# Kernel tuning notes

Measured on AMD Instinct MI355X. Metric: run time of the kernel, lower is better.

## Reference

```python
import jax, jax.numpy as jnp
import numpy as np

B = 8192
N = 1024


def euler_to_matrix_xyz(e):
    # e: [B,3] angles; R = Rx(a) @ Ry(b) @ Rz(c) (pytorch3d 'XYZ' convention)
    a, b, c = e[..., 0], e[..., 1], e[..., 2]
    ca, sa = jnp.cos(a), jnp.sin(a)
    cb, sb = jnp.cos(b), jnp.sin(b)
    cc, sc = jnp.cos(c), jnp.sin(c)
    one = jnp.ones_like(a)
    zero = jnp.zeros_like(a)
    Rx = jnp.stack([one, zero, zero,
                    zero, ca, -sa,
                    zero, sa, ca], axis=-1).reshape(-1, 3, 3)
    Ry = jnp.stack([cb, zero, sb,
                    zero, one, zero,
                    -sb, zero, cb], axis=-1).reshape(-1, 3, 3)
    Rz = jnp.stack([cc, -sc, zero,
                    sc, cc, zero,
                    zero, zero, one], axis=-1).reshape(-1, 3, 3)
    return jnp.einsum('bij,bjk->bik', Rx, jnp.einsum('bij,bjk->bik', Ry, Rz))


def manifold2euler(manifold, mode):
    m1, m2, m3, m4 = (manifold[:, 0], manifold[:, 1], manifold[:, 2], manifold[:, 3])
    sgn = jnp.where(mode > 0.5, 1.0, -1.0)
    euler2 = sgn * jnp.arcsin(jnp.sqrt(m3 ** 2 / (m1 ** 2 + m2 ** 2 + m3 ** 2)))
    euler3 = jnp.arctan2(m4, m3 / (jnp.sin(euler2) + 1e-9))
    tmp = jnp.cos(euler2) * jnp.cos(euler3)
    euler1 = jnp.arctan2(m2 / tmp, m1 / tmp)
    euler3 = jnp.where(euler3 > 0, euler3, euler3 + 2 * np.pi)
    return jnp.stack([euler1, euler2, euler3], axis=-1)


def setup_inputs() -> dict:
    key = jax.random.key(0)
    k1, k2, k3, k4 = jax.random.split(key, 4)
    return {
        'pred': jax.random.normal(k1, (B, 4), dtype=jnp.float32),
        'mode': jax.random.uniform(k2, (B,), dtype=jnp.float32),
        'gt': jax.random.normal(k3, (B, 3), dtype=jnp.float32),
        'point': jax.random.normal(k4, (B, N, 3), dtype=jnp.float32),
    }


def reference(pred, mode, gt, point):
    euler_pred = manifold2euler(pred, mode)          # [B,3]
    rm_gt = euler_to_matrix_xyz(gt)                  # [B,3,3]
    rm_pred = euler_to_matrix_xyz(euler_pred)        # [B,3,3]
    # original: row-vector point [*,1,3] @ R [*,3,3]; R depends only on batch
    point_gt = jnp.einsum('bnj,bjk->bnk', point, rm_gt)
    point_pred = jnp.einsum('bnj,bjk->bnk', point, rm_pred)
    diff = point_pred - point_gt                     # [B,N,3]
    dist = jnp.linalg.norm(diff, axis=-1)            # [B,N]
    return jnp.mean(dist)
```

## Files before the change

### kernel.cpp

```cpp
#include <hip/hip_runtime.h>
#include <math.h>

constexpr int B_ = 8192;
constexpr int N_ = 1024;
constexpr int NTHREADS = 256;
constexpr int BATCHES_PER_BLOCK = 4;
constexpr int NBLOCKS = B_ / BATCHES_PER_BLOCK;

__device__ __forceinline__ void euler_to_mat(float a, float b, float c, float R[9]) {
    float ca = cosf(a), sa = sinf(a);
    float cb = cosf(b), sb = sinf(b);
    float cc = cosf(c), sc = sinf(c);
    R[0] = cb * cc;             R[1] = -cb * sc;            R[2] = sb;
    R[3] = ca * sc + sa * sb * cc; R[4] = ca * cc - sa * sb * sc; R[5] = -sa * cb;
    R[6] = sa * sc - ca * sb * cc; R[7] = sa * cc + ca * sb * sc; R[8] = ca * cb;
}

__global__ __launch_bounds__(NTHREADS)
void add_loss_kernel(const float* __restrict__ pred,
                     const float* __restrict__ mode,
                     const float* __restrict__ gt,
                     const float* __restrict__ point,
                     float* __restrict__ out)
{
    __shared__ float sM[9];
    __shared__ float spts[N_ * 3];
    __shared__ float swave[NTHREADS / 64];

    const int tid = threadIdx.x;
    float local = 0.0f;

    for (int ib = 0; ib < BATCHES_PER_BLOCK; ++ib) {
        const int b = blockIdx.x * BATCHES_PER_BLOCK + ib;

        const float4* gp = (const float4*)(point + (size_t)b * (N_ * 3));
        float4* sp4 = (float4*)spts;
        #pragma unroll
        for (int i = 0; i < (N_ * 3 / 4) / NTHREADS; ++i)
            sp4[tid + NTHREADS * i] = gp[tid + NTHREADS * i];

        if (tid == 0) {
            float m1 = pred[b * 4 + 0], m2 = pred[b * 4 + 1];
            float m3 = pred[b * 4 + 2], m4 = pred[b * 4 + 3];
            float sgn = (mode[b] > 0.5f) ? 1.0f : -1.0f;
            float e2 = sgn * asinf(sqrtf(m3 * m3 / (m1 * m1 + m2 * m2 + m3 * m3)));
            float e3 = atan2f(m4, m3 / (sinf(e2) + 1e-9f));
            float tmp = cosf(e2) * cosf(e3);
            float e1 = atan2f(m2 / tmp, m1 / tmp);
            e3 = (e3 > 0.0f) ? e3 : (e3 + 6.2831854820251465f);
            float P[9], G[9];
            euler_to_mat(e1, e2, e3, P);
            euler_to_mat(gt[b * 3 + 0], gt[b * 3 + 1], gt[b * 3 + 2], G);
            #pragma unroll
            for (int i = 0; i < 9; ++i) sM[i] = P[i] - G[i];
        }
        __syncthreads();

        const float M0 = sM[0], M1 = sM[1], M2 = sM[2];
        const float M3 = sM[3], M4 = sM[4], M5 = sM[5];
        const float M6 = sM[6], M7 = sM[7], M8 = sM[8];

        #pragma unroll
        for (int i = 0; i < N_ / NTHREADS; ++i) {
            int n = tid + NTHREADS * i;
            float px = spts[3 * n + 0], py = spts[3 * n + 1], pz = spts[3 * n + 2];
            float dx = px * M0 + py * M3 + pz * M6;
            float dy = px * M1 + py * M4 + pz * M7;
            float dz = px * M2 + py * M5 + pz * M8;
            local += sqrtf(dx * dx + dy * dy + dz * dz);
        }
        __syncthreads();
    }

    #pragma unroll
    for (int off = 32; off > 0; off >>= 1)
        local += __shfl_down(local, off, 64);
    if ((tid & 63) == 0) swave[tid >> 6] = local;
    __syncthreads();
    if (tid == 0) {
        float s = swave[0] + swave[1] + swave[2] + swave[3];
        atomicAdd(out, s * (1.0f / ((float)B_ * (float)N_)));
    }
}

extern "C" void kernel_launch(void* const* d_in, const int* in_sizes, int n_in,
                              void* d_out, int out_size, void* d_ws, size_t ws_size,
                              hipStream_t stream) {
    const float* pred  = (const float*)d_in[0];
    const float* mode  = (const float*)d_in[1];
    const float* gt    = (const float*)d_in[2];
    const float* point = (const float*)d_in[3];
    float* out = (float*)d_out;

    hipMemsetAsync(out, 0, sizeof(float), stream);
    add_loss_kernel<<<NBLOCKS, NTHREADS, 0, stream>>>(pred, mode, gt, point, out);
}
```

Before: 171.2 us.

## Split rotation prep, per-batch point kernel, and deterministic two-stage reduction

Moves the per-batch rotation-difference matrix computation into a separate fully parallel prep kernel, so it no longer runs serially on one thread per block while the others wait. The point kernel now assigns one batch per block and loads points straight into registers as three float4 per thread, removing the shared-memory staging and its extra barriers. The global atomic is replaced by per-block partial sums and a single-block final reduction. This adds two extra kernel launches and a workspace round trip, and keeps a fused fallback for when the workspace is too small.

```diff
diff --git a/kernel.cpp b/kernel.cpp
--- a/kernel.cpp
+++ b/kernel.cpp
@@ -4,83 +4,132 @@
 constexpr int B_ = 8192;
 constexpr int N_ = 1024;
 constexpr int NTHREADS = 256;
-constexpr int BATCHES_PER_BLOCK = 4;
-constexpr int NBLOCKS = B_ / BATCHES_PER_BLOCK;
+constexpr float SCALE = 1.0f / ((float)B_ * (float)N_);
 
 __device__ __forceinline__ void euler_to_mat(float a, float b, float c, float R[9]) {
     float ca = cosf(a), sa = sinf(a);
     float cb = cosf(b), sb = sinf(b);
     float cc = cosf(c), sc = sinf(c);
-    R[0] = cb * cc;             R[1] = -cb * sc;            R[2] = sb;
+    R[0] = cb * cc;                R[1] = -cb * sc;               R[2] = sb;
     R[3] = ca * sc + sa * sb * cc; R[4] = ca * cc - sa * sb * sc; R[5] = -sa * cb;
     R[6] = sa * sc - ca * sb * cc; R[7] = sa * cc + ca * sb * sc; R[8] = ca * cb;
 }
 
+__device__ __forceinline__ void compute_M(const float* __restrict__ pred,
+                                          const float* __restrict__ mode,
+                                          const float* __restrict__ gt,
+                                          int b, float M[9]) {
+    float m1 = pred[b * 4 + 0], m2 = pred[b * 4 + 1];
+    float m3 = pred[b * 4 + 2], m4 = pred[b * 4 + 3];
+    float sgn = (mode[b] > 0.5f) ? 1.0f : -1.0f;
+    float e2 = sgn * asinf(sqrtf(m3 * m3 / (m1 * m1 + m2 * m2 + m3 * m3)));
+    float e3 = atan2f(m4, m3 / (sinf(e2) + 1e-9f));
+    float tmp = cosf(e2) * cosf(e3);
+    float e1 = atan2f(m2 / tmp, m1 / tmp);
+    e3 = (e3 > 0.0f) ? e3 : (e3 + 6.2831854820251465f);
+    float P[9], G[9];
+    euler_to_mat(e1, e2, e3, P);
+    euler_to_mat(gt[b * 3 + 0], gt[b * 3 + 1], gt[b * 3 + 2], G);
+    #pragma unroll
+    for (int i = 0; i < 9; ++i) M[i] = P[i] - G[i];
+}
+
+__global__ __launch_bounds__(256)
+void prep_M_kernel(const float* __restrict__ pred, const float* __restrict__ mode,
+                   const float* __restrict__ gt, float* __restrict__ Mout) {
+    int b = blockIdx.x * blockDim.x + threadIdx.x;
+    if (b >= B_) return;
+    float M[9];
+    compute_M(pred, mode, gt, b, M);
+    #pragma unroll
+    for (int i = 0; i < 9; ++i) Mout[b * 9 + i] = M[i];
+}
+
+__device__ __forceinline__ float dist3(float px, float py, float pz, const float M[9]) {
+    float dx = px * M[0] + py * M[3] + pz * M[6];
+    float dy = px * M[1] + py * M[4] + pz * M[7];
+    float dz = px * M[2] + py * M[5] + pz * M[8];
+    return sqrtf(dx * dx + dy * dy + dz * dz);
+}
+
 __global__ __launch_bounds__(NTHREADS)
-void add_loss_kernel(const float* __restrict__ pred,
-                     const float* __restrict__ mode,
-                     const float* __restrict__ gt,
-                     const float* __restrict__ point,
-                     float* __restrict__ out)
+void point_kernel(const float* __restrict__ point,
+                  const float* __restrict__ Mg,
+                  float* __restrict__ partial)
 {
+    const int b = blockIdx.x;
+    const int t = threadIdx.x;
     __shared__ float sM[9];
-    __shared__ float spts[N_ * 3];
     __shared__ float swave[NTHREADS / 64];
 
-    const int tid = threadIdx.x;
-    float local = 0.0f;
+    if (t < 9) sM[t] = Mg[b * 9 + t];
+    __syncthreads();
+    float M[9];
+    #pragma unroll
+    for (int i = 0; i < 9; ++i) M[i] = sM[i];
 
-    for (int ib = 0; ib < BATCHES_PER_BLOCK; ++ib) {
-        const int b = blockIdx.x * BATCHES_PER_BLOCK + ib;
+    const float4* gp = (const float4*)(point + (size_t)b * (N_ * 3));
+    float4 p0 = gp[3 * t + 0];
+    float4 p1 = gp[3 * t + 1];
+    float4 p2 = gp[3 * t + 2];
 
-        const float4* gp = (const float4*)(point + (size_t)b * (N_ * 3));
-        float4* sp4 = (float4*)spts;
-        #pragma unroll
-        for (int i = 0; i < (N_ * 3 / 4) / NTHREADS; ++i)
-            sp4[tid + NTHREADS * i] = gp[tid + NTHREADS * i];
-
-        if (tid == 0) {
-            float m1 = pred[b * 4 + 0], m2 = pred[b * 4 + 1];
-            float m3 = pred[b * 4 + 2], m4 = pred[b * 4 + 3];
-            float sgn = (mode[b] > 0.5f) ? 1.0f : -1.0f;
-            float e2 = sgn * asinf(sqrtf(m3 * m3 / (m1 * m1 + m2 * m2 + m3 * m3)));
-            float e3 = atan2f(m4, m3 / (sinf(e2) + 1e-9f));
-            float tmp = cosf(e2) * cosf(e3);
-            float e1 = atan2f(m2 / tmp, m1 / tmp);
-            e3 = (e3 > 0.0f) ? e3 : (e3 + 6.2831854820251465f);
-            float P[9], G[9];
-            euler_to_mat(e1, e2, e3, P);
-            euler_to_mat(gt[b * 3 + 0], gt[b * 3 + 1], gt[b * 3 + 2], G);
-            #pragma unroll
-            for (int i = 0; i < 9; ++i) sM[i] = P[i] - G[i];
-        }
-        __syncthreads();
-
-        const float M0 = sM[0], M1 = sM[1], M2 = sM[2];
-        const float M3 = sM[3], M4 = sM[4], M5 = sM[5];
-        const float M6 = sM[6], M7 = sM[7], M8 = sM[8];
-
-        #pragma unroll
-        for (int i = 0; i < N_ / NTHREADS; ++i) {
-            int n = tid + NTHREADS * i;
-            float px = spts[3 * n + 0], py = spts[3 * n + 1], pz = spts[3 * n + 2];
-            float dx = px * M0 + py * M3 + pz * M6;
-            float dy = px * M1 + py * M4 + pz * M7;
-            float dz = px * M2 + py * M5 + pz * M8;
-            local += sqrtf(dx * dx + dy * dy + dz * dz);
-        }
-        __syncthreads();
-    }
+    float local = dist3(p0.x, p0.y, p0.z, M)
+                + dist3(p0.w, p1.x, p1.y, M)
+                + dist3(p1.z, p1.w, p2.x, M)
+                + dist3(p2.y, p2.z, p2.w, M);
 
     #pragma unroll
     for (int off = 32; off > 0; off >>= 1)
         local += __shfl_down(local, off, 64);
-    if ((tid & 63) == 0) swave[tid >> 6] = local;
+    if ((t & 63) == 0) swave[t >> 6] = local;
     __syncthreads();
-    if (tid == 0) {
-        float s = swave[0] + swave[1] + swave[2] + swave[3];
-        atomicAdd(out, s * (1.0f / ((float)B_ * (float)N_)));
+    if (t == 0) partial[b] = swave[0] + swave[1] + swave[2] + swave[3];
+}
+
+__global__ __launch_bounds__(1024)
+void reduce_kernel(const float* __restrict__ partial, float* __restrict__ out) {
+    __shared__ float swave[1024 / 64];
+    const int t = threadIdx.x;
+    float local = 0.0f;
+    #pragma unroll
+    for (int i = 0; i < B_ / 1024; ++i) local += partial[t + 1024 * i];
+    #pragma unroll
+    for (int off = 32; off > 0; off >>= 1)
+        local += __shfl_down(local, off, 64);
+    if ((t & 63) == 0) swave[t >> 6] = local;
+    __syncthreads();
+    if (t == 0) {
+        float s = 0.0f;
+        #pragma unroll
+        for (int i = 0; i < 1024 / 64; ++i) s += swave[i];
+        out[0] = s * SCALE;
     }
+}
+
+__global__ __launch_bounds__(NTHREADS)
+void fused_kernel(const float* __restrict__ pred, const float* __restrict__ mode,
+                  const float* __restrict__ gt, const float* __restrict__ point,
+                  float* __restrict__ out) {
+    const int b = blockIdx.x;
+    const int t = threadIdx.x;
+    __shared__ float swave[NTHREADS / 64];
+    float M[9];
+    compute_M(pred, mode, gt, b, M);
+    const float4* gp = (const float4*)(point + (size_t)b * (N_ * 3));
+    float4 p0 = gp[3 * t + 0];
+    float4 p1 = gp[3 * t + 1];
+    float4 p2 = gp[3 * t + 2];
+    float local = dist3(p0.x, p0.y, p0.z, M)
+                + dist3(p0.w, p1.x, p1.y, M)
+                + dist3(p1.z, p1.w, p2.x, M)
+                + dist3(p2.y, p2.z, p2.w, M);
+    #pragma unroll
+    for (int off = 32; off > 0; off >>= 1)
+        local += __shfl_down(local, off, 64);
+    if ((t & 63) == 0) swave[t >> 6] = local;
+    __syncthreads();
+    if (t == 0)
+        atomicAdd(out, (swave[0] + swave[1] + swave[2] + swave[3]) * SCALE);
 }
 
 extern "C" void kernel_launch(void* const* d_in, const int* in_sizes, int n_in,
@@ -92,6 +141,15 @@
     const float* point = (const float*)d_in[3];
     float* out = (float*)d_out;
 
-    hipMemsetAsync(out, 0, sizeof(float), stream);
-    add_loss_kernel<<<NBLOCKS, NTHREADS, 0, stream>>>(pred, mode, gt, point, out);
+    const size_t need = (size_t)(B_ * 9 + B_) * sizeof(float);
+    if (ws_size >= need) {
+        float* Mg      = (float*)d_ws;
+        float* partial = Mg + B_ * 9;
+        prep_M_kernel<<<B_ / 256, 256, 0, stream>>>(pred, mode, gt, Mg);
+        point_kernel<<<B_, NTHREADS, 0, stream>>>(point, Mg, partial);
+        reduce_kernel<<<1, 1024, 0, stream>>>(partial, out);
+    } else {
+        hipMemsetAsync(out, 0, sizeof(float), stream);
+        fused_kernel<<<B_, NTHREADS, 0, stream>>>(pred, mode, gt, point, out);
+    }
 }
```

Result: faster. 153.8 us (-10.1%).
